# Optimization experiments

Hardware: AMD Instinct MI355X
Metric: run time of the kernel (lower is better)

The kernel has to match this reference:

```python
import jax, jax.numpy as jnp
import numpy as np

N, E = 50000, 800000
IN, HID, H, OUT, ED = 128, 16, 4, 7, 2
HC = HID * H  # 64


def setup_inputs() -> dict:
    key = jax.random.key(0)
    ks = jax.random.split(key, 24)
    g = lambda k, s, sc=0.05: (jax.random.normal(k, s, dtype=jnp.float32) * sc)
    return {
        'x': g(ks[0], (N, IN), 1.0),
        'edge_attr': g(ks[1], (E, ED), 1.0),
        'edge_index': jax.random.randint(ks[2], (2, E), 0, N),
        # conv1: in=IN, out=HID, heads=H, edge_dim=ED, concat=True
        'Wq1': g(ks[3], (IN, HC)), 'bq1': jnp.zeros((HC,), jnp.float32),
        'Wk1': g(ks[4], (IN, HC)), 'bk1': jnp.zeros((HC,), jnp.float32),
        'Wv1': g(ks[5], (IN, HC)), 'bv1': jnp.zeros((HC,), jnp.float32),
        'We1': g(ks[6], (ED, HC)),  # lin_edge has no bias in PyG
        'Ws1': g(ks[7], (IN, HC)), 'bs1': jnp.zeros((HC,), jnp.float32),
        # conv2: in=HC, out=OUT, heads=1, concat=False
        'Wq2': g(ks[8], (HC, OUT)), 'bq2': jnp.zeros((OUT,), jnp.float32),
        'Wk2': g(ks[9], (HC, OUT)), 'bk2': jnp.zeros((OUT,), jnp.float32),
        'Wv2': g(ks[10], (HC, OUT)), 'bv2': jnp.zeros((OUT,), jnp.float32),
        'Ws2': g(ks[11], (HC, OUT)), 'bs2': jnp.zeros((OUT,), jnp.float32),
    }


def transformer_conv(x, src, dst, Wq, bq, Wk, bk, Wv, bv, Ws, bs,
                     heads, ch, concat, edge_attr=None, We=None):
    """PyG TransformerConv (eval mode, root_weight=True, beta=False)."""
    n = x.shape[0]
    q = (x @ Wq + bq).reshape(n, heads, ch)
    k = (x @ Wk + bk).reshape(n, heads, ch)
    v = (x @ Wv + bv).reshape(n, heads, ch)
    kj = k[src]  # [E,H,C] gather from source nodes
    vj = v[src]
    if We is not None:
        e = (edge_attr @ We).reshape(-1, heads, ch)
        kj = kj + e
        vj = vj + e
    # per-edge attention logits [E,H]
    alpha = (q[dst] * kj).sum(-1) / jnp.sqrt(jnp.float32(ch))
    # scatter-softmax over incoming edges of each destination node
    amax = jax.ops.segment_max(alpha, dst, num_segments=n)
    ex = jnp.exp(alpha - amax[dst])
    denom = jax.ops.segment_sum(ex, dst, num_segments=n)
    a = ex / jnp.maximum(denom, 1e-16)[dst]
    out = jax.ops.segment_sum(vj * a[:, :, None], dst, num_segments=n)  # [N,H,C]
    out = out.reshape(n, heads * ch) if concat else out.mean(axis=1)
    return out + x @ Ws + bs  # skip connection (lin_skip)


def reference(x, edge_attr, edge_index, Wq1, bq1, Wk1, bk1, Wv1, bv1, We1,
              Ws1, bs1, Wq2, bq2, Wk2, bk2, Wv2, bv2, Ws2, bs2):
    src, dst = edge_index[0], edge_index[1]
    # eval mode: feature/attention dropout are identity
    h = transformer_conv(x, src, dst, Wq1, bq1, Wk1, bk1, Wv1, bv1, Ws1, bs1,
                         H, HID, True, edge_attr=edge_attr, We=We1)
    h = jax.nn.elu(h)
    out = transformer_conv(h, src, dst, Wq2, bq2, Wk2, bk2, Wv2, bv2, Ws2, bs2,
                           1, OUT, False)
    return out
```

## Files before the change

kernel.cpp:

```cpp
#include <hip/hip_runtime.h>


#define N_NODES 50000
#define N_EDGES 800000
#define IN_F    128
#define HC      64
#define NH      4
#define CH      16
#define OUTF    7

#define DPB 100
#define NBK (N_NODES / DPB)
#define SC_EPB 4096
#define SCA_BLOCKS ((N_EDGES + SC_EPB - 1) / SC_EPB)
#define P1_BLOCKS (N_NODES / 16)

typedef __attribute__((ext_vector_type(8))) short bf16x8;
typedef __attribute__((ext_vector_type(4))) float f32x4;

__device__ __forceinline__ unsigned short f2bf(float f) {
    unsigned u = __float_as_uint(f);
    unsigned r = u + 0x7FFFu + ((u >> 16) & 1u);
    return (unsigned short)(r >> 16);
}
__device__ __forceinline__ float bflo(unsigned u) { return __uint_as_float(u << 16); }
__device__ __forceinline__ float bfhi(unsigned u) { return __uint_as_float(u & 0xFFFF0000u); }
__device__ __forceinline__ float elu_fast(float x) {
    return x > 0.f ? x : __expf(x) - 1.f;
}

__device__ __forceinline__ float dpp_add4(float x) {
    int t;
    t = __builtin_amdgcn_update_dpp(0, __float_as_int(x), 0xB1, 0xF, 0xF, false);
    x += __int_as_float(t);
    t = __builtin_amdgcn_update_dpp(0, __float_as_int(x), 0x4E, 0xF, 0xF, false);
    x += __int_as_float(t);
    return x;
}
__device__ __forceinline__ float dpp_add16(float x) {
    int t;
    t = __builtin_amdgcn_update_dpp(0, __float_as_int(x), 0xB1, 0xF, 0xF, false);
    x += __int_as_float(t);
    t = __builtin_amdgcn_update_dpp(0, __float_as_int(x), 0x4E, 0xF, 0xF, false);
    x += __int_as_float(t);
    t = __builtin_amdgcn_update_dpp(0, __float_as_int(x), 0x124, 0xF, 0xF, false);
    x += __int_as_float(t);
    t = __builtin_amdgcn_update_dpp(0, __float_as_int(x), 0x128, 0xF, 0xF, false);
    x += __int_as_float(t);
    return x;
}
__device__ __forceinline__ float dpp_max16(float x) {
    int t;
    t = __builtin_amdgcn_update_dpp(0, __float_as_int(x), 0xB1, 0xF, 0xF, false);
    x = fmaxf(x, __int_as_float(t));
    t = __builtin_amdgcn_update_dpp(0, __float_as_int(x), 0x4E, 0xF, 0xF, false);
    x = fmaxf(x, __int_as_float(t));
    t = __builtin_amdgcn_update_dpp(0, __float_as_int(x), 0x124, 0xF, 0xF, false);
    x = fmaxf(x, __int_as_float(t));
    t = __builtin_amdgcn_update_dpp(0, __float_as_int(x), 0x128, 0xF, 0xF, false);
    x = fmaxf(x, __int_as_float(t));
    return x;
}

__global__ __launch_bounds__(256) void convert_w_kernel(
    const float* __restrict__ Wq, const float* __restrict__ Wk,
    const float* __restrict__ Wv, const float* __restrict__ Ws,
    unsigned short* __restrict__ Wt, int* __restrict__ bcnt)
{
    int i = blockIdx.x * 256 + threadIdx.x;
    if (blockIdx.x < 2) {
        int j = blockIdx.x * 256 + threadIdx.x;
        if (j < NBK) bcnt[j] = 0;
    }
    if (i >= 4 * HC * IN_F) return;
    int m   = i >> 13;
    int col = (i >> 7) & 63;
    int k   = i & 127;
    const float* W = (m == 0) ? Wq : (m == 1) ? Wk : (m == 2) ? Wv : Ws;
    Wt[i] = f2bf(W[k * HC + col]);
}

__global__ __launch_bounds__(256) void bhist_kernel(
    const int* __restrict__ ei, int* __restrict__ bcnt)
{
    __shared__ int cnt[NBK];
    const int t = threadIdx.x;
    const int e0 = blockIdx.x * SC_EPB;
    const int e1 = (e0 + SC_EPB < N_EDGES) ? e0 + SC_EPB : N_EDGES;
    for (int j = t; j < NBK; j += 256) cnt[j] = 0;
    __syncthreads();
    for (int e = e0 + t; e < e1; e += 256)
        atomicAdd(&cnt[ei[N_EDGES + e] / DPB], 1);
    __syncthreads();
    for (int j = t; j < NBK; j += 256)
        if (cnt[j]) atomicAdd(&bcnt[j], cnt[j]);
}

__global__ __launch_bounds__(256) void bscan_kernel(
    const int* __restrict__ bcnt, int* __restrict__ bofs2, int* __restrict__ bcur)
{
    __shared__ int partial[256];
    const int t = threadIdx.x;
    const int b0 = t * 2;
    int c0 = (b0     < NBK) ? bcnt[b0]     : 0;
    int c1 = (b0 + 1 < NBK) ? bcnt[b0 + 1] : 0;
    int s = c0 + c1;
    partial[t] = s;
    __syncthreads();
    for (int d = 1; d < 256; d <<= 1) {
        int u = (t >= d) ? partial[t - d] : 0;
        __syncthreads();
        partial[t] += u;
        __syncthreads();
    }
    int run = partial[t] - s;
    if (b0 < NBK)     { bofs2[b0]     = run;      bcur[b0]     = run; }
    if (b0 + 1 < NBK) { bofs2[b0 + 1] = run + c0; bcur[b0 + 1] = run + c0; }
    if (t == 255) bofs2[NBK] = N_EDGES;
}

__global__ __launch_bounds__(256) void proj1_scatterA_kernel(
    const float* __restrict__ x, const unsigned short* __restrict__ Wt,
    const float* __restrict__ bq, const float* __restrict__ bk,
    const float* __restrict__ bv, const float* __restrict__ bs,
    float* __restrict__ q1, unsigned short* __restrict__ kv1,
    float* __restrict__ s1,
    const int* __restrict__ ei, const float* __restrict__ ea,
    int* __restrict__ bcur, uint2* __restrict__ etmp)
{
    __shared__ unsigned short xs[16][136];
    __shared__ int cnt[NBK];
    __shared__ int base[NBK];
    const int t = threadIdx.x;

    if (blockIdx.x >= P1_BLOCKS) {
        const int e0 = (blockIdx.x - P1_BLOCKS) * SC_EPB;
        const int e1 = (e0 + SC_EPB < N_EDGES) ? e0 + SC_EPB : N_EDGES;
        for (int j = t; j < NBK; j += 256) cnt[j] = 0;
        __syncthreads();
        for (int e = e0 + t; e < e1; e += 256)
            atomicAdd(&cnt[ei[N_EDGES + e] / DPB], 1);
        __syncthreads();
        for (int j = t; j < NBK; j += 256) {
            int c = cnt[j];
            if (c) base[j] = atomicAdd(&bcur[j], c);
            cnt[j] = 0;
        }
        __syncthreads();
        for (int e = e0 + t; e < e1; e += 256) {
            int d = ei[N_EDGES + e];
            int s = ei[e];
            int b = d / DPB;
            int li = atomicAdd(&cnt[b], 1);
            uint2 r;
            r.x = (unsigned)s | ((unsigned)d << 16);
            r.y = (unsigned)f2bf(ea[(size_t)e * 2])
                | ((unsigned)f2bf(ea[(size_t)e * 2 + 1]) << 16);
            etmp[base[b] + li] = r;
        }
        return;
    }

    const int w = t >> 6, lane = t & 63;
    const int n0 = blockIdx.x * 16;
    const int col16 = lane & 15, kg = lane >> 4;

    bf16x8 bfrag[4][4];
#pragma unroll
    for (int tt = 0; tt < 4; tt++) {
        const unsigned short* bp = Wt + ((size_t)(w * 64 + tt * 16 + col16) * IN_F) + 8 * kg;
#pragma unroll
        for (int kc = 0; kc < 4; kc++)
            bfrag[kc][tt] = *(const bf16x8*)(bp + kc * 32);
    }

    {
        int row = t >> 4, k8 = (t & 15) * 8;
        const float* xp = x + (size_t)(n0 + row) * IN_F + k8;
        float4 f0 = *(const float4*)xp;
        float4 f1 = *(const float4*)(xp + 4);
        uint4 pk;
        pk.x = f2bf(f0.x) | ((unsigned)f2bf(f0.y) << 16);
        pk.y = f2bf(f0.z) | ((unsigned)f2bf(f0.w) << 16);
        pk.z = f2bf(f1.x) | ((unsigned)f2bf(f1.y) << 16);
        pk.w = f2bf(f1.z) | ((unsigned)f2bf(f1.w) << 16);
        *(uint4*)&xs[row][k8] = pk;
    }
    __syncthreads();

    f32x4 acc[4] = { {0,0,0,0}, {0,0,0,0}, {0,0,0,0}, {0,0,0,0} };
#pragma unroll
    for (int kc = 0; kc < 4; kc++) {
        bf16x8 a = *(const bf16x8*)&xs[col16][kc * 32 + 8 * kg];
#pragma unroll
        for (int tt = 0; tt < 4; tt++)
            acc[tt] = __builtin_amdgcn_mfma_f32_16x16x32_bf16(a, bfrag[kc][tt], acc[tt], 0, 0, 0);
    }

    if (w == 0 || w == 3) {
        const float* Bm = (w == 0) ? bq : bs;
        float*       Om = (w == 0) ? q1 : s1;
#pragma unroll
        for (int tt = 0; tt < 4; tt++) {
            int col = tt * 16 + col16;
            float bias = Bm[col];
#pragma unroll
            for (int r = 0; r < 4; r++) {
                int node = n0 + kg * 4 + r;
                Om[(size_t)node * HC + col] = acc[tt][r] + bias;
            }
        }
    } else {
        const float* Bm = (w == 1) ? bk : bv;
        const int cbase = (w == 1) ? 0 : 64;
#pragma unroll
        for (int tt = 0; tt < 4; tt++) {
            int col = tt * 16 + col16;
            float bias = Bm[col];
#pragma unroll
            for (int r = 0; r < 4; r++) {
                int node = n0 + kg * 4 + r;
                kv1[(size_t)node * 128 + cbase + col] = f2bf(acc[tt][r] + bias);
            }
        }
    }
}

__global__ __launch_bounds__(256) void sortB_kernel(
    const int* __restrict__ bofs2, const uint2* __restrict__ etmp,
    uint2* __restrict__ erec, int* __restrict__ offs)
{
    __shared__ int deg[DPB];
    __shared__ int pre[DPB];
    __shared__ int cur[DPB];
    const int t = threadIdx.x;
    const int b = blockIdx.x;
    const int dlo = b * DPB;
    const int rbeg = bofs2[b], rend = bofs2[b + 1];

    if (t < DPB) deg[t] = 0;
    __syncthreads();
    for (int i = rbeg + t; i < rend; i += 256)
        atomicAdd(&deg[(int)(etmp[i].x >> 16) - dlo], 1);
    __syncthreads();
    if (t < DPB) pre[t] = deg[t];
    __syncthreads();
#pragma unroll
    for (int d = 1; d < DPB; d <<= 1) {
        int u = (t >= d && t < DPB) ? pre[t - d] : 0;
        __syncthreads();
        if (t < DPB) pre[t] += u;
        __syncthreads();
    }
    if (t < DPB) {
        int o = rbeg + pre[t] - deg[t];
        offs[dlo + t] = o;
        cur[t] = o;
    }
    if (b == NBK - 1 && t == 0) offs[N_NODES] = N_EDGES;
    __syncthreads();
    for (int i = rbeg + t; i < rend; i += 256) {
        uint2 r = etmp[i];
        int d = (int)(r.x >> 16) - dlo;
        int pos = atomicAdd(&cur[d], 1);
        uint2 o;
        o.x = r.x & 0xFFFFu;
        o.y = r.y;
        erec[pos] = o;
    }
}

__global__ __launch_bounds__(256) void attn1_kernel(
    const int* __restrict__ offs, const uint2* __restrict__ erec,
    const float* __restrict__ We,
    const float* __restrict__ q1, const unsigned short* __restrict__ kv1,
    const float* __restrict__ s1, float* __restrict__ h)
{
    int n    = (blockIdx.x * 256 + threadIdx.x) >> 6;
    int lane = threadIdx.x & 63;
    if (n >= N_NODES) return;
    const int g = lane >> 4;
    const int s = lane & 15;

    const float4 qv  = *(const float4*)(q1 + (size_t)n * HC + s * 4);
    const float4 We0 = *(const float4*)(We + s * 4);
    const float4 We1 = *(const float4*)(We + HC + s * 4);

    float qw0 = dpp_add4(qv.x*We0.x + qv.y*We0.y + qv.z*We0.z + qv.w*We0.w);
    float qw1 = dpp_add4(qv.x*We1.x + qv.y*We1.y + qv.z*We1.z + qv.w*We1.w);

    const int beg = offs[n], end = offs[n + 1];
    float m = -3.402823466e38f, l = 0.f, A0 = 0.f, A1 = 0.f;
    float4 acc = make_float4(0.f, 0.f, 0.f, 0.f);

    for (int base = beg; base < end; base += 4) {
        int i = base + g;
        bool valid = (i < end);
        uint2 r = erec[valid ? i : beg];
        int src = (int)r.x;
        float ea0 = bflo(r.y), ea1 = bfhi(r.y);
        const unsigned short* kvp = kv1 + ((size_t)src << 7) + (s << 2);
        uint2 kraw = *(const uint2*)kvp;
        uint2 vraw = *(const uint2*)(kvp + 64);
        float k0 = bflo(kraw.x), k1 = bfhi(kraw.x);
        float k2 = bflo(kraw.y), k3 = bfhi(kraw.y);
        float dot = qv.x*k0 + qv.y*k1 + qv.z*k2 + qv.w*k3;
        dot = dpp_add4(dot);
        float logit = valid ? (dot + ea0 * qw0 + ea1 * qw1) * 0.25f
                            : -3.402823466e38f;
        if (__any(logit > m + 8.f)) {
            float mn = fmaxf(m, logit);
            float sm = __expf(m - mn);
            l *= sm; A0 *= sm; A1 *= sm;
            acc.x *= sm; acc.y *= sm; acc.z *= sm; acc.w *= sm;
            m = mn;
        }
        float pe = valid ? __expf(logit - m) : 0.f;
        l += pe;
        float v0 = bflo(vraw.x), v1 = bfhi(vraw.x);
        float v2 = bflo(vraw.y), v3 = bfhi(vraw.y);
        acc.x += pe * v0; acc.y += pe * v1;
        acc.z += pe * v2; acc.w += pe * v3;
        A0 += pe * ea0;  A1 += pe * ea1;
    }

    if (end > beg) {
        float M = fmaxf(m, __shfl_xor(m, 16));
        M = fmaxf(M, __shfl_xor(M, 32));
        float sc = __expf(m - M);
        l *= sc; A0 *= sc; A1 *= sc;
        acc.x *= sc; acc.y *= sc; acc.z *= sc; acc.w *= sc;
        l  += __shfl_xor(l, 16);   l  += __shfl_xor(l, 32);
        A0 += __shfl_xor(A0, 16);  A0 += __shfl_xor(A0, 32);
        A1 += __shfl_xor(A1, 16);  A1 += __shfl_xor(A1, 32);
        acc.x += __shfl_xor(acc.x, 16); acc.x += __shfl_xor(acc.x, 32);
        acc.y += __shfl_xor(acc.y, 16); acc.y += __shfl_xor(acc.y, 32);
        acc.z += __shfl_xor(acc.z, 16); acc.z += __shfl_xor(acc.z, 32);
        acc.w += __shfl_xor(acc.w, 16); acc.w += __shfl_xor(acc.w, 32);
        if (lane < 16) {
            float inv = 1.f / l;
            float4 sk = *(const float4*)(s1 + (size_t)n * HC + s * 4);
            float4 o;
            o.x = elu_fast((acc.x + A0 * We0.x + A1 * We1.x) * inv + sk.x);
            o.y = elu_fast((acc.y + A0 * We0.y + A1 * We1.y) * inv + sk.y);
            o.z = elu_fast((acc.z + A0 * We0.z + A1 * We1.z) * inv + sk.z);
            o.w = elu_fast((acc.w + A0 * We0.w + A1 * We1.w) * inv + sk.w);
            *(float4*)(h + (size_t)n * HC + s * 4) = o;
        }
    } else if (lane < 16) {
        float4 sk = *(const float4*)(s1 + (size_t)n * HC + s * 4);
        float4 o;
        o.x = elu_fast(sk.x);
        o.y = elu_fast(sk.y);
        o.z = elu_fast(sk.z);
        o.w = elu_fast(sk.w);
        *(float4*)(h + (size_t)n * HC + s * 4) = o;
    }
}

__global__ __launch_bounds__(256) void proj2_kernel(
    const float* __restrict__ h,
    const float* __restrict__ Wq, const float* __restrict__ bq,
    const float* __restrict__ Wk, const float* __restrict__ bk,
    const float* __restrict__ Wv, const float* __restrict__ bv,
    const float* __restrict__ Ws, const float* __restrict__ bs,
    float* __restrict__ q2p, float* __restrict__ kv2, float* __restrict__ s2p)
{
    __shared__ float Wsm[HC][4][8];
    __shared__ float Bsm[4][8];
    const int t = threadIdx.x;

    for (int j = t; j < HC * 28; j += 256) {
        int i = j / 28, r = j % 28, mtx = r / 7, c = r % 7;
        const float* W = (mtx == 0) ? Wq : (mtx == 1) ? Wk : (mtx == 2) ? Wv : Ws;
        Wsm[i][mtx][c] = W[i * OUTF + c];
    }
    for (int j = t; j < HC * 4; j += 256)
        Wsm[j >> 2][j & 3][7] = 0.f;
    if (t < 32) {
        int mtx = t >> 3, c = t & 7;
        const float* B = (mtx == 0) ? bq : (mtx == 1) ? bk : (mtx == 2) ? bv : bs;
        Bsm[mtx][c] = (c < 7) ? B[c] : 0.f;
    }
    __syncthreads();

    int n = blockIdx.x * 256 + t;
    if (n >= N_NODES) return;

    float acc[4][8];
#pragma unroll
    for (int mtx = 0; mtx < 4; mtx++)
#pragma unroll
        for (int c = 0; c < 8; c++) acc[mtx][c] = Bsm[mtx][c];

    const float4* hp = (const float4*)(h + (size_t)n * HC);
#pragma unroll 4
    for (int i4 = 0; i4 < 16; i4++) {
        float4 hv = hp[i4];
        float hx[4] = { hv.x, hv.y, hv.z, hv.w };
#pragma unroll
        for (int e = 0; e < 4; e++) {
            int i = i4 * 4 + e;
#pragma unroll
            for (int mtx = 0; mtx < 4; mtx++) {
                float4 wa = *(const float4*)&Wsm[i][mtx][0];
                float4 wb = *(const float4*)&Wsm[i][mtx][4];
                acc[mtx][0] += hx[e] * wa.x; acc[mtx][1] += hx[e] * wa.y;
                acc[mtx][2] += hx[e] * wa.z; acc[mtx][3] += hx[e] * wa.w;
                acc[mtx][4] += hx[e] * wb.x; acc[mtx][5] += hx[e] * wb.y;
                acc[mtx][6] += hx[e] * wb.z; acc[mtx][7] += hx[e] * wb.w;
            }
        }
    }

    float4* q2v = (float4*)(q2p + (size_t)n * 8);
    q2v[0] = make_float4(acc[0][0], acc[0][1], acc[0][2], acc[0][3]);
    q2v[1] = make_float4(acc[0][4], acc[0][5], acc[0][6], acc[0][7]);
    float4* kvv = (float4*)(kv2 + (size_t)n * 16);
    kvv[0] = make_float4(acc[1][0], acc[1][1], acc[1][2], acc[1][3]);
    kvv[1] = make_float4(acc[1][4], acc[1][5], acc[1][6], acc[1][7]);
    kvv[2] = make_float4(acc[2][0], acc[2][1], acc[2][2], acc[2][3]);
    kvv[3] = make_float4(acc[2][4], acc[2][5], acc[2][6], acc[2][7]);
    float4* s2v = (float4*)(s2p + (size_t)n * 8);
    s2v[0] = make_float4(acc[3][0], acc[3][1], acc[3][2], acc[3][3]);
    s2v[1] = make_float4(acc[3][4], acc[3][5], acc[3][6], acc[3][7]);
}

__global__ __launch_bounds__(256) void attn2_kernel(
    const int* __restrict__ offs, const uint2* __restrict__ erec,
    const float* __restrict__ q2p, const float* __restrict__ kv2,
    const float* __restrict__ s2p, float* __restrict__ out)
{
    int idx = blockIdx.x * 256 + threadIdx.x;
    int n   = idx >> 4;
    int s   = idx & 15;
    if (n >= N_NODES) return;

    float4 qa = *(const float4*)(q2p + (size_t)n * 8);
    float4 qb = *(const float4*)(q2p + (size_t)n * 8 + 4);
    int beg = offs[n], end = offs[n + 1];

    float m = -3.402823466e38f, l = 0.f, a[OUTF];
#pragma unroll
    for (int c = 0; c < OUTF; c++) a[c] = 0.f;

    for (int i = beg + s; i < end; i += 16) {
        int src = (int)erec[i].x;
        const float4* kvp = (const float4*)(kv2 + (size_t)src * 16);
        float4 ka = kvp[0], kb = kvp[1], va = kvp[2], vb = kvp[3];
        float dot = qa.x * ka.x + qa.y * ka.y + qa.z * ka.z + qa.w * ka.w
                  + qb.x * kb.x + qb.y * kb.y + qb.z * kb.z;
        float logit = dot * 0.37796447300922725f;
        float mn = fmaxf(m, logit);
        float sc = __expf(m - mn);
        float pe = __expf(logit - mn);
        l = l * sc + pe;
        a[0] = a[0] * sc + pe * va.x;
        a[1] = a[1] * sc + pe * va.y;
        a[2] = a[2] * sc + pe * va.z;
        a[3] = a[3] * sc + pe * va.w;
        a[4] = a[4] * sc + pe * vb.x;
        a[5] = a[5] * sc + pe * vb.y;
        a[6] = a[6] * sc + pe * vb.z;
        m = mn;
    }

    if (end > beg) {
        float M = dpp_max16(m);
        float sc = __expf(m - M);
        l *= sc;
#pragma unroll
        for (int c = 0; c < OUTF; c++) a[c] *= sc;
        l = dpp_add16(l);
#pragma unroll
        for (int c = 0; c < OUTF; c++) a[c] = dpp_add16(a[c]);
        if (s == 0) {
            float inv = 1.f / fmaxf(l, 1e-16f);
#pragma unroll
            for (int c = 0; c < OUTF; c++)
                out[(size_t)n * OUTF + c] = a[c] * inv + s2p[(size_t)n * 8 + c];
        }
    } else if (s == 0) {
#pragma unroll
        for (int c = 0; c < OUTF; c++)
            out[(size_t)n * OUTF + c] = s2p[(size_t)n * 8 + c];
    }
}

extern "C" void kernel_launch(void* const* d_in, const int* in_sizes, int n_in,
                              void* d_out, int out_size, void* d_ws, size_t ws_size,
                              hipStream_t stream)
{
    const float* x    = (const float*)d_in[0];
    const float* ea   = (const float*)d_in[1];
    const int*   ei   = (const int*)d_in[2];
    const float* Wq1  = (const float*)d_in[3];
    const float* bq1  = (const float*)d_in[4];
    const float* Wk1  = (const float*)d_in[5];
    const float* bk1  = (const float*)d_in[6];
    const float* Wv1  = (const float*)d_in[7];
    const float* bv1  = (const float*)d_in[8];
    const float* We1  = (const float*)d_in[9];
    const float* Ws1  = (const float*)d_in[10];
    const float* bs1  = (const float*)d_in[11];
    const float* Wq2  = (const float*)d_in[12];
    const float* bq2  = (const float*)d_in[13];
    const float* Wk2  = (const float*)d_in[14];
    const float* bk2  = (const float*)d_in[15];
    const float* Wv2  = (const float*)d_in[16];
    const float* bv2  = (const float*)d_in[17];
    const float* Ws2  = (const float*)d_in[18];
    const float* bs2  = (const float*)d_in[19];
    float* out = (float*)d_out;

    float* ws = (float*)d_ws;
    float*          q1  = ws;
    float*          s1  = q1 + (size_t)N_NODES * HC;
    unsigned short* kv1 = (unsigned short*)(s1 + (size_t)N_NODES * HC);
    float*          hbuf = q1;
    uint2* erec = (uint2*)((float*)kv1 + (size_t)N_NODES * HC);
    uint2* etmp = erec + N_EDGES;
    float*  q2p  = (float*)(etmp + N_EDGES);
    float*  kv2  = q2p + (size_t)N_NODES * 8;
    float*  s2p  = kv2 + (size_t)N_NODES * 16;
    unsigned short* Wt = (unsigned short*)(s2p + (size_t)N_NODES * 8);
    int*    offs  = (int*)(Wt + 4 * HC * IN_F);
    int*    bcnt  = offs + N_NODES + 1;
    int*    bofs2 = bcnt + NBK;
    int*    bcur  = bofs2 + NBK + 1;

    convert_w_kernel<<<(4 * HC * IN_F + 255) / 256, 256, 0, stream>>>(
        Wq1, Wk1, Wv1, Ws1, Wt, bcnt);

    bhist_kernel<<<SCA_BLOCKS, 256, 0, stream>>>(ei, bcnt);
    bscan_kernel<<<1, 256, 0, stream>>>(bcnt, bofs2, bcur);

    proj1_scatterA_kernel<<<P1_BLOCKS + SCA_BLOCKS, 256, 0, stream>>>(
        x, Wt, bq1, bk1, bv1, bs1, q1, kv1, s1, ei, ea, bcur, etmp);

    sortB_kernel<<<NBK, 256, 0, stream>>>(bofs2, etmp, erec, offs);

    attn1_kernel<<<(N_NODES * 64 + 255) / 256, 256, 0, stream>>>(
        offs, erec, We1, q1, kv1, s1, hbuf);

    proj2_kernel<<<(N_NODES + 255) / 256, 256, 0, stream>>>(
        hbuf, Wq2, bq2, Wk2, bk2, Wv2, bv2, Ws2, bs2, q2p, kv2, s2p);

    attn2_kernel<<<(N_NODES * 16 + 255) / 256, 256, 0, stream>>>(
        offs, erec, q2p, kv2, s2p, out);
}
```

Baseline: 145.6 us.

## Store q1/s1 in bf16, double proj1 tile size, schedule scatter blocks first

The layer-1 query and skip projections are now stored as bf16 instead of fp32, and the attention kernel unpacks them. This halves their write and read traffic. The projection tile grows from 16 to 32 nodes per block, so each block reuses the loaded weight fragments across two MFMA row tiles, with bounds guards for the tail. The edge scatter blocks now come first in the grid so they start early. The cost is lower precision on q and the skip term, and more registers per thread from the doubled accumulators.

```diff
diff --git a/kernel.cpp b/kernel.cpp
--- a/kernel.cpp
+++ b/kernel.cpp
@@ -13,7 +13,8 @@
 #define NBK (N_NODES / DPB)
 #define SC_EPB 4096
 #define SCA_BLOCKS ((N_EDGES + SC_EPB - 1) / SC_EPB)
-#define P1_BLOCKS (N_NODES / 16)
+#define P1_TILE 32
+#define P1_BLOCKS ((N_NODES + P1_TILE - 1) / P1_TILE)
 
 typedef __attribute__((ext_vector_type(8))) short bf16x8;
 typedef __attribute__((ext_vector_type(4))) float f32x4;
@@ -123,18 +124,18 @@
     const float* __restrict__ x, const unsigned short* __restrict__ Wt,
     const float* __restrict__ bq, const float* __restrict__ bk,
     const float* __restrict__ bv, const float* __restrict__ bs,
-    float* __restrict__ q1, unsigned short* __restrict__ kv1,
-    float* __restrict__ s1,
+    unsigned short* __restrict__ q1b, unsigned short* __restrict__ kv1,
+    unsigned short* __restrict__ s1b,
     const int* __restrict__ ei, const float* __restrict__ ea,
     int* __restrict__ bcur, uint2* __restrict__ etmp)
 {
-    __shared__ unsigned short xs[16][136];
+    __shared__ unsigned short xs[P1_TILE][136];
     __shared__ int cnt[NBK];
     __shared__ int base[NBK];
     const int t = threadIdx.x;
 
-    if (blockIdx.x >= P1_BLOCKS) {
-        const int e0 = (blockIdx.x - P1_BLOCKS) * SC_EPB;
+    if (blockIdx.x < SCA_BLOCKS) {
+        const int e0 = blockIdx.x * SC_EPB;
         const int e1 = (e0 + SC_EPB < N_EDGES) ? e0 + SC_EPB : N_EDGES;
         for (int j = t; j < NBK; j += 256) cnt[j] = 0;
         __syncthreads();
@@ -162,7 +163,7 @@
     }
 
     const int w = t >> 6, lane = t & 63;
-    const int n0 = blockIdx.x * 16;
+    const int n0 = (blockIdx.x - SCA_BLOCKS) * P1_TILE;
     const int col16 = lane & 15, kg = lane >> 4;
 
     bf16x8 bfrag[4][4];
@@ -175,52 +176,71 @@
     }
 
     {
-        int row = t >> 4, k8 = (t & 15) * 8;
-        const float* xp = x + (size_t)(n0 + row) * IN_F + k8;
-        float4 f0 = *(const float4*)xp;
-        float4 f1 = *(const float4*)(xp + 4);
-        uint4 pk;
-        pk.x = f2bf(f0.x) | ((unsigned)f2bf(f0.y) << 16);
-        pk.y = f2bf(f0.z) | ((unsigned)f2bf(f0.w) << 16);
-        pk.z = f2bf(f1.x) | ((unsigned)f2bf(f1.y) << 16);
-        pk.w = f2bf(f1.z) | ((unsigned)f2bf(f1.w) << 16);
-        *(uint4*)&xs[row][k8] = pk;
-    }
-    __syncthreads();
-
-    f32x4 acc[4] = { {0,0,0,0}, {0,0,0,0}, {0,0,0,0}, {0,0,0,0} };
+        int row = t >> 3, cg = (t & 7) * 16;
+        uint4 pk0 = make_uint4(0, 0, 0, 0), pk1 = make_uint4(0, 0, 0, 0);
+        if (n0 + row < N_NODES) {
+            const float* xp = x + (size_t)(n0 + row) * IN_F + cg;
+            float4 f0 = *(const float4*)xp;
+            float4 f1 = *(const float4*)(xp + 4);
+            float4 f2 = *(const float4*)(xp + 8);
+            float4 f3 = *(const float4*)(xp + 12);
+            pk0.x = f2bf(f0.x) | ((unsigned)f2bf(f0.y) << 16);
+            pk0.y = f2bf(f0.z) | ((unsigned)f2bf(f0.w) << 16);
+            pk0.z = f2bf(f1.x) | ((unsigned)f2bf(f1.y) << 16);
+            pk0.w = f2bf(f1.z) | ((unsigned)f2bf(f1.w) << 16);
+            pk1.x = f2bf(f2.x) | ((unsigned)f2bf(f2.y) << 16);
+            pk1.y = f2bf(f2.z) | ((unsigned)f2bf(f2.w) << 16);
+            pk1.z = f2bf(f3.x) | ((unsigned)f2bf(f3.y) << 16);
+            pk1.w = f2bf(f3.z) | ((unsigned)f2bf(f3.w) << 16);
+        }
+        *(uint4*)&xs[row][cg]     = pk0;
+        *(uint4*)&xs[row][cg + 8] = pk1;
+    }
+    __syncthreads();
+
+    f32x4 acc[2][4] = { { {0,0,0,0}, {0,0,0,0}, {0,0,0,0}, {0,0,0,0} },
+                        { {0,0,0,0}, {0,0,0,0}, {0,0,0,0}, {0,0,0,0} } };
 #pragma unroll
     for (int kc = 0; kc < 4; kc++) {
-        bf16x8 a = *(const bf16x8*)&xs[col16][kc * 32 + 8 * kg];
-#pragma unroll
-        for (int tt = 0; tt < 4; tt++)
-            acc[tt] = __builtin_amdgcn_mfma_f32_16x16x32_bf16(a, bfrag[kc][tt], acc[tt], 0, 0, 0);
+        bf16x8 a0 = *(const bf16x8*)&xs[col16][kc * 32 + 8 * kg];
+        bf16x8 a1 = *(const bf16x8*)&xs[16 + col16][kc * 32 + 8 * kg];
+#pragma unroll
+        for (int tt = 0; tt < 4; tt++) {
+            acc[0][tt] = __builtin_amdgcn_mfma_f32_16x16x32_bf16(a0, bfrag[kc][tt], acc[0][tt], 0, 0, 0);
+            acc[1][tt] = __builtin_amdgcn_mfma_f32_16x16x32_bf16(a1, bfrag[kc][tt], acc[1][tt], 0, 0, 0);
+        }
     }
 
     if (w == 0 || w == 3) {
         const float* Bm = (w == 0) ? bq : bs;
-        float*       Om = (w == 0) ? q1 : s1;
+        unsigned short* Om = (w == 0) ? q1b : s1b;
+#pragma unroll
+        for (int mt = 0; mt < 2; mt++)
 #pragma unroll
         for (int tt = 0; tt < 4; tt++) {
             int col = tt * 16 + col16;
             float bias = Bm[col];
 #pragma unroll
             for (int r = 0; r < 4; r++) {
-                int node = n0 + kg * 4 + r;
-                Om[(size_t)node * HC + col] = acc[tt][r] + bias;
+                int node = n0 + mt * 16 + kg * 4 + r;
+                if (node < N_NODES)
+                    Om[(size_t)node * HC + col] = f2bf(acc[mt][tt][r] + bias);
             }
         }
     } else {
         const float* Bm = (w == 1) ? bk : bv;
         const int cbase = (w == 1) ? 0 : 64;
 #pragma unroll
+        for (int mt = 0; mt < 2; mt++)
+#pragma unroll
         for (int tt = 0; tt < 4; tt++) {
             int col = tt * 16 + col16;
             float bias = Bm[col];
 #pragma unroll
             for (int r = 0; r < 4; r++) {
-                int node = n0 + kg * 4 + r;
-                kv1[(size_t)node * 128 + cbase + col] = f2bf(acc[tt][r] + bias);
+                int node = n0 + mt * 16 + kg * 4 + r;
+                if (node < N_NODES)
+                    kv1[(size_t)node * 128 + cbase + col] = f2bf(acc[mt][tt][r] + bias);
             }
         }
     }
@@ -273,8 +293,8 @@
 __global__ __launch_bounds__(256) void attn1_kernel(
     const int* __restrict__ offs, const uint2* __restrict__ erec,
     const float* __restrict__ We,
-    const float* __restrict__ q1, const unsigned short* __restrict__ kv1,
-    const float* __restrict__ s1, float* __restrict__ h)
+    const unsigned short* __restrict__ q1b, const unsigned short* __restrict__ kv1,
+    const unsigned short* __restrict__ s1b, float* __restrict__ h)
 {
     int n    = (blockIdx.x * 256 + threadIdx.x) >> 6;
     int lane = threadIdx.x & 63;
@@ -282,7 +302,9 @@
     const int g = lane >> 4;
     const int s = lane & 15;
 
-    const float4 qv  = *(const float4*)(q1 + (size_t)n * HC + s * 4);
+    uint2 qraw = *(const uint2*)(q1b + ((size_t)n << 6) + (s << 2));
+    const float4 qv = make_float4(bflo(qraw.x), bfhi(qraw.x),
+                                  bflo(qraw.y), bfhi(qraw.y));
     const float4 We0 = *(const float4*)(We + s * 4);
     const float4 We1 = *(const float4*)(We + HC + s * 4);
 
@@ -339,21 +361,21 @@
         acc.w += __shfl_xor(acc.w, 16); acc.w += __shfl_xor(acc.w, 32);
         if (lane < 16) {
             float inv = 1.f / l;
-            float4 sk = *(const float4*)(s1 + (size_t)n * HC + s * 4);
+            uint2 sraw = *(const uint2*)(s1b + ((size_t)n << 6) + (s << 2));
             float4 o;
-            o.x = elu_fast((acc.x + A0 * We0.x + A1 * We1.x) * inv + sk.x);
-            o.y = elu_fast((acc.y + A0 * We0.y + A1 * We1.y) * inv + sk.y);
-            o.z = elu_fast((acc.z + A0 * We0.z + A1 * We1.z) * inv + sk.z);
-            o.w = elu_fast((acc.w + A0 * We0.w + A1 * We1.w) * inv + sk.w);
+            o.x = elu_fast((acc.x + A0 * We0.x + A1 * We1.x) * inv + bflo(sraw.x));
+            o.y = elu_fast((acc.y + A0 * We0.y + A1 * We1.y) * inv + bfhi(sraw.x));
+            o.z = elu_fast((acc.z + A0 * We0.z + A1 * We1.z) * inv + bflo(sraw.y));
+            o.w = elu_fast((acc.w + A0 * We0.w + A1 * We1.w) * inv + bfhi(sraw.y));
             *(float4*)(h + (size_t)n * HC + s * 4) = o;
         }
     } else if (lane < 16) {
-        float4 sk = *(const float4*)(s1 + (size_t)n * HC + s * 4);
+        uint2 sraw = *(const uint2*)(s1b + ((size_t)n << 6) + (s << 2));
         float4 o;
-        o.x = elu_fast(sk.x);
-        o.y = elu_fast(sk.y);
-        o.z = elu_fast(sk.z);
-        o.w = elu_fast(sk.w);
+        o.x = elu_fast(bflo(sraw.x));
+        o.y = elu_fast(bfhi(sraw.x));
+        o.z = elu_fast(bflo(sraw.y));
+        o.w = elu_fast(bfhi(sraw.y));
         *(float4*)(h + (size_t)n * HC + s * 4) = o;
     }
 }
@@ -513,13 +535,12 @@
     const float* bs2  = (const float*)d_in[19];
     float* out = (float*)d_out;
 
-    float* ws = (float*)d_ws;
-    float*          q1  = ws;
-    float*          s1  = q1 + (size_t)N_NODES * HC;
-    unsigned short* kv1 = (unsigned short*)(s1 + (size_t)N_NODES * HC);
-    float*          hbuf = q1;
-    uint2* erec = (uint2*)((float*)kv1 + (size_t)N_NODES * HC);
-    uint2* etmp = erec + N_EDGES;
+    unsigned short* q1b = (unsigned short*)d_ws;
+    unsigned short* s1b = q1b + (size_t)N_NODES * HC;
+    unsigned short* kv1 = s1b + (size_t)N_NODES * HC;
+    float*  hbuf = (float*)(kv1 + (size_t)N_NODES * 128);
+    uint2*  erec = (uint2*)(hbuf + (size_t)N_NODES * HC);
+    uint2*  etmp = erec + N_EDGES;
     float*  q2p  = (float*)(etmp + N_EDGES);
     float*  kv2  = q2p + (size_t)N_NODES * 8;
     float*  s2p  = kv2 + (size_t)N_NODES * 16;
@@ -535,13 +556,13 @@
     bhist_kernel<<<SCA_BLOCKS, 256, 0, stream>>>(ei, bcnt);
     bscan_kernel<<<1, 256, 0, stream>>>(bcnt, bofs2, bcur);
 
-    proj1_scatterA_kernel<<<P1_BLOCKS + SCA_BLOCKS, 256, 0, stream>>>(
-        x, Wt, bq1, bk1, bv1, bs1, q1, kv1, s1, ei, ea, bcur, etmp);
+    proj1_scatterA_kernel<<<SCA_BLOCKS + P1_BLOCKS, 256, 0, stream>>>(
+        x, Wt, bq1, bk1, bv1, bs1, q1b, kv1, s1b, ei, ea, bcur, etmp);
 
     sortB_kernel<<<NBK, 256, 0, stream>>>(bofs2, etmp, erec, offs);
 
     attn1_kernel<<<(N_NODES * 64 + 255) / 256, 256, 0, stream>>>(
-        offs, erec, We1, q1, kv1, s1, hbuf);
+        offs, erec, We1, q1b, kv1, s1b, hbuf);
 
     proj2_kernel<<<(N_NODES + 255) / 256, 256, 0, stream>>>(
         hbuf, Wq2, bq2, Wk2, bk2, Wv2, bv2, Ws2, bs2, q2p, kv2, s2p);
```

Result: faster. 135.6 us, median of 3 (-6.9%).
